# Performance work log

Hardware: AMD Instinct MI355X
Metric: run time of the kernel (lower is better)

Reference implementation:

```python
import jax, jax.numpy as jnp
import numpy as np

IN_FEATURES = 8192
OUT_FEATURES = 8192
MAX_STATES = 100
THRESHOLD = MAX_STATES // 2  # 50
TRACE_DECAY = 0.8


def setup_inputs() -> dict:
    key = jax.random.key(0)
    k1, k2 = jax.random.split(key)
    # binary spike input in {0,1}
    spike_input = (jax.random.uniform(k1, (1, IN_FEATURES)) < 0.5).astype(jnp.float32)
    # synapse states initialized around the threshold, as in the torch buffer init
    synapse_states = jax.random.randint(
        k2, (OUT_FEATURES, IN_FEATURES), THRESHOLD - 5, THRESHOLD + 5
    ).astype(jnp.float32)
    membrane_potential = jnp.zeros((OUT_FEATURES,), jnp.float32)
    adaptive_threshold = jnp.ones((OUT_FEATURES,), jnp.float32)
    eligibility_trace = jnp.zeros((OUT_FEATURES, IN_FEATURES), jnp.float32)
    return {
        "spike_input": spike_input,
        "synapse_states": synapse_states,
        "membrane_potential": membrane_potential,
        "adaptive_threshold": adaptive_threshold,
        "eligibility_trace": eligibility_trace,
    }


def reference(spike_input, synapse_states, membrane_potential, adaptive_threshold, eligibility_trace):
    # ternary (binary) weight mask from synapse states
    w = (synapse_states > THRESHOLD).astype(jnp.float32)  # [out, in]
    x = spike_input.reshape(1, -1)                         # [1, in]
    # current = x @ w^T, flattened to [out] (batch must be 1)
    current = jnp.einsum("bi,oi->bo", x, w).reshape(-1)    # [out]
    # LIF membrane update
    v_mem = membrane_potential * 0.7 + current             # [out]
    spikes = (v_mem >= adaptive_threshold).astype(jnp.float32)
    # eligibility trace: decay + outer-product update
    new_trace = eligibility_trace * TRACE_DECAY + jnp.outer(spikes, x.reshape(-1))
    # post-spike reset with soft decay
    new_v_mem = v_mem * (1.0 - spikes) * 0.5
    return spikes, new_v_mem, new_trace
```

## Files before the change

### kernel.cpp

```cpp
#include <hip/hip_runtime.h>


#define IN_F 8192
#define OUT_F 8192
#define THR_F 50.0f
#define BLOCK 256
#define V4_PER_THREAD 8

typedef float f4 __attribute__((ext_vector_type(4)));

__global__ __launch_bounds__(BLOCK) void snn_fused_kernel(
    const float* __restrict__ x,
    const float* __restrict__ syn,
    const float* __restrict__ vmem_in,
    const float* __restrict__ thr,
    const float* __restrict__ trace_in,
    float* __restrict__ out_spikes,
    float* __restrict__ out_vmem,
    float* __restrict__ out_trace)
{
    const int o = blockIdx.x;
    const int tid = threadIdx.x;
    const size_t rowoff = (size_t)o * IN_F;

    const f4* __restrict__ syn4 = reinterpret_cast<const f4*>(syn + rowoff);
    const f4* __restrict__ x4   = reinterpret_cast<const f4*>(x);
    const f4* __restrict__ tr4  = reinterpret_cast<const f4*>(trace_in + rowoff);
    f4* __restrict__ ot4        = reinterpret_cast<f4*>(out_trace + rowoff);

    f4 tr[V4_PER_THREAD];
#pragma unroll
    for (int j = 0; j < V4_PER_THREAD; ++j) {
        const int idx = tid + j * BLOCK;
        tr[j] = __builtin_nontemporal_load(&tr4[idx]);
    }

    float partial = 0.0f;
#pragma unroll
    for (int j = 0; j < V4_PER_THREAD; ++j) {
        const int idx = tid + j * BLOCK;
        const f4 s  = syn4[idx];
        const f4 xv = x4[idx];
        partial += (s.x > THR_F) ? xv.x : 0.0f;
        partial += (s.y > THR_F) ? xv.y : 0.0f;
        partial += (s.z > THR_F) ? xv.z : 0.0f;
        partial += (s.w > THR_F) ? xv.w : 0.0f;
    }

#pragma unroll
    for (int off = 32; off > 0; off >>= 1)
        partial += __shfl_down(partial, off, 64);

    __shared__ float wsum[BLOCK / 64];
    __shared__ float s_spike;
    const int wid = tid >> 6;
    const int lane = tid & 63;
    if (lane == 0) wsum[wid] = partial;
    __syncthreads();

    if (tid == 0) {
        const float cur = wsum[0] + wsum[1] + wsum[2] + wsum[3];
        const float v = vmem_in[o] * 0.7f + cur;
        const float sp = (v >= thr[o]) ? 1.0f : 0.0f;
        out_spikes[o] = sp;
        out_vmem[o] = v * (1.0f - sp) * 0.5f;
        s_spike = sp;
    }
    __syncthreads();
    const float sp = s_spike;

#pragma unroll
    for (int j = 0; j < V4_PER_THREAD; ++j) {
        const int idx = tid + j * BLOCK;
        const f4 xv = x4[idx];
        f4 r;
        r.x = tr[j].x * 0.8f + sp * xv.x;
        r.y = tr[j].y * 0.8f + sp * xv.y;
        r.z = tr[j].z * 0.8f + sp * xv.z;
        r.w = tr[j].w * 0.8f + sp * xv.w;
        __builtin_nontemporal_store(r, &ot4[idx]);
    }
}

extern "C" void kernel_launch(void* const* d_in, const int* in_sizes, int n_in,
                              void* d_out, int out_size, void* d_ws, size_t ws_size,
                              hipStream_t stream) {
    const float* x     = (const float*)d_in[0];
    const float* syn   = (const float*)d_in[1];
    const float* vmem  = (const float*)d_in[2];
    const float* thr   = (const float*)d_in[3];
    const float* trace = (const float*)d_in[4];

    float* out = (float*)d_out;
    float* out_spikes = out;
    float* out_vmem   = out + OUT_F;
    float* out_trace  = out + 2 * OUT_F;

    snn_fused_kernel<<<OUT_F, BLOCK, 0, stream>>>(
        x, syn, vmem, thr, trace, out_spikes, out_vmem, out_trace);
}
```

Measured before the change: 119.0 us.

## Assign one output row per wavefront and stream trace in chunks

Each wavefront now handles a whole output row instead of a block per row. This removes the shared-memory reduction and both block barriers, using an xor shuffle and a lane-0 broadcast instead. Synapse loads become nontemporal and run in chunks. Only the first trace chunk is prefetched before the spike decision, and the rest is streamed afterwards to keep register use down. Each wave now carries more serial work per row and fewer memory requests are in flight before the reduction.

```diff
diff --git a/kernel.cpp b/kernel.cpp
--- a/kernel.cpp
+++ b/kernel.cpp
@@ -5,11 +5,13 @@
 #define OUT_F 8192
 #define THR_F 50.0f
 #define BLOCK 256
-#define V4_PER_THREAD 8
+#define WAVES_PER_BLOCK 4
+#define CHUNK 8
+#define NCHUNK 4
 
 typedef float f4 __attribute__((ext_vector_type(4)));
 
-__global__ __launch_bounds__(BLOCK) void snn_fused_kernel(
+__global__ __launch_bounds__(BLOCK) void snn_wave_kernel(
     const float* __restrict__ x,
     const float* __restrict__ syn,
     const float* __restrict__ vmem_in,
@@ -19,8 +21,9 @@
     float* __restrict__ out_vmem,
     float* __restrict__ out_trace)
 {
-    const int o = blockIdx.x;
-    const int tid = threadIdx.x;
+    const int wid  = threadIdx.x >> 6;
+    const int lane = threadIdx.x & 63;
+    const int o    = blockIdx.x * WAVES_PER_BLOCK + wid;
     const size_t rowoff = (size_t)o * IN_F;
 
     const f4* __restrict__ syn4 = reinterpret_cast<const f4*>(syn + rowoff);
@@ -28,57 +31,73 @@
     const f4* __restrict__ tr4  = reinterpret_cast<const f4*>(trace_in + rowoff);
     f4* __restrict__ ot4        = reinterpret_cast<f4*>(out_trace + rowoff);
 
-    f4 tr[V4_PER_THREAD];
+    float partial = 0.0f;
 #pragma unroll
-    for (int j = 0; j < V4_PER_THREAD; ++j) {
-        const int idx = tid + j * BLOCK;
-        tr[j] = __builtin_nontemporal_load(&tr4[idx]);
+    for (int c = 0; c < NCHUNK; ++c) {
+        f4 s[CHUNK], xv[CHUNK];
+#pragma unroll
+        for (int j = 0; j < CHUNK; ++j) {
+            const int idx = lane + (c * CHUNK + j) * 64;
+            s[j]  = __builtin_nontemporal_load(&syn4[idx]);
+            xv[j] = x4[idx];
+        }
+#pragma unroll
+        for (int j = 0; j < CHUNK; ++j) {
+            partial += (s[j].x > THR_F) ? xv[j].x : 0.0f;
+            partial += (s[j].y > THR_F) ? xv[j].y : 0.0f;
+            partial += (s[j].z > THR_F) ? xv[j].z : 0.0f;
+            partial += (s[j].w > THR_F) ? xv[j].w : 0.0f;
+        }
     }
 
-    float partial = 0.0f;
+    f4 tpre[CHUNK];
 #pragma unroll
-    for (int j = 0; j < V4_PER_THREAD; ++j) {
-        const int idx = tid + j * BLOCK;
-        const f4 s  = syn4[idx];
-        const f4 xv = x4[idx];
-        partial += (s.x > THR_F) ? xv.x : 0.0f;
-        partial += (s.y > THR_F) ? xv.y : 0.0f;
-        partial += (s.z > THR_F) ? xv.z : 0.0f;
-        partial += (s.w > THR_F) ? xv.w : 0.0f;
-    }
+    for (int j = 0; j < CHUNK; ++j)
+        tpre[j] = __builtin_nontemporal_load(&tr4[lane + j * 64]);
 
 #pragma unroll
     for (int off = 32; off > 0; off >>= 1)
-        partial += __shfl_down(partial, off, 64);
+        partial += __shfl_xor(partial, off, 64);
 
-    __shared__ float wsum[BLOCK / 64];
-    __shared__ float s_spike;
-    const int wid = tid >> 6;
-    const int lane = tid & 63;
-    if (lane == 0) wsum[wid] = partial;
-    __syncthreads();
-
-    if (tid == 0) {
-        const float cur = wsum[0] + wsum[1] + wsum[2] + wsum[3];
-        const float v = vmem_in[o] * 0.7f + cur;
-        const float sp = (v >= thr[o]) ? 1.0f : 0.0f;
+    float sp;
+    if (lane == 0) {
+        const float v = vmem_in[o] * 0.7f + partial;
+        sp = (v >= thr[o]) ? 1.0f : 0.0f;
         out_spikes[o] = sp;
-        out_vmem[o] = v * (1.0f - sp) * 0.5f;
-        s_spike = sp;
+        out_vmem[o]   = v * (1.0f - sp) * 0.5f;
     }
-    __syncthreads();
-    const float sp = s_spike;
+    sp = __shfl(sp, 0, 64);
 
 #pragma unroll
-    for (int j = 0; j < V4_PER_THREAD; ++j) {
-        const int idx = tid + j * BLOCK;
+    for (int j = 0; j < CHUNK; ++j) {
+        const int idx = lane + j * 64;
         const f4 xv = x4[idx];
         f4 r;
-        r.x = tr[j].x * 0.8f + sp * xv.x;
-        r.y = tr[j].y * 0.8f + sp * xv.y;
-        r.z = tr[j].z * 0.8f + sp * xv.z;
-        r.w = tr[j].w * 0.8f + sp * xv.w;
+        r.x = tpre[j].x * 0.8f + sp * xv.x;
+        r.y = tpre[j].y * 0.8f + sp * xv.y;
+        r.z = tpre[j].z * 0.8f + sp * xv.z;
+        r.w = tpre[j].w * 0.8f + sp * xv.w;
         __builtin_nontemporal_store(r, &ot4[idx]);
+    }
+#pragma unroll
+    for (int c = 1; c < NCHUNK; ++c) {
+        f4 t[CHUNK], xv[CHUNK];
+#pragma unroll
+        for (int j = 0; j < CHUNK; ++j) {
+            const int idx = lane + (c * CHUNK + j) * 64;
+            t[j]  = __builtin_nontemporal_load(&tr4[idx]);
+            xv[j] = x4[idx];
+        }
+#pragma unroll
+        for (int j = 0; j < CHUNK; ++j) {
+            const int idx = lane + (c * CHUNK + j) * 64;
+            f4 r;
+            r.x = t[j].x * 0.8f + sp * xv[j].x;
+            r.y = t[j].y * 0.8f + sp * xv[j].y;
+            r.z = t[j].z * 0.8f + sp * xv[j].z;
+            r.w = t[j].w * 0.8f + sp * xv[j].w;
+            __builtin_nontemporal_store(r, &ot4[idx]);
+        }
     }
 }
 
@@ -96,6 +115,6 @@
     float* out_vmem   = out + OUT_F;
     float* out_trace  = out + 2 * OUT_F;
 
-    snn_fused_kernel<<<OUT_F, BLOCK, 0, stream>>>(
+    snn_wave_kernel<<<OUT_F / WAVES_PER_BLOCK, BLOCK, 0, stream>>>(
         x, syn, vmem, thr, trace, out_spikes, out_vmem, out_trace);
 }
```

New measurement: 134.6 us. 1.13x slower.

## Software-pipeline rows so trace update of row r-1 overlaps dot of row r

Applied to the files above, without the earlier changes.

Each block now processes four output rows and, in each step, interleaves the dot product for row r with the trace decay-and-update for row r-1, reusing the spike computed in the previous step. Grid size drops by four and the per-block serial phase (dot, then barrier, then trace) is replaced by a skewed pipeline, so trace loads and stores run alongside synapse loads. Every thread now reads the reduced spike from a double-buffered shared array instead of thread 0 broadcasting it. The catch is fewer blocks, plus trace loads that are no longer nontemporal and no longer issued ahead in registers.

```diff
diff --git a/kernel.cpp b/kernel.cpp
--- a/kernel.cpp
+++ b/kernel.cpp
@@ -5,11 +5,12 @@
 #define OUT_F 8192
 #define THR_F 50.0f
 #define BLOCK 256
-#define V4_PER_THREAD 8
+#define RPB 4
+#define NCHUNK 8
 
 typedef float f4 __attribute__((ext_vector_type(4)));
 
-__global__ __launch_bounds__(BLOCK) void snn_fused_kernel(
+__global__ __launch_bounds__(BLOCK) void snn_pipe_kernel(
     const float* __restrict__ x,
     const float* __restrict__ syn,
     const float* __restrict__ vmem_in,
@@ -19,66 +20,67 @@
     float* __restrict__ out_vmem,
     float* __restrict__ out_trace)
 {
-    const int o = blockIdx.x;
-    const int tid = threadIdx.x;
-    const size_t rowoff = (size_t)o * IN_F;
+    const int tid  = threadIdx.x;
+    const int base = blockIdx.x * RPB;
+    const f4* __restrict__ x4 = reinterpret_cast<const f4*>(x);
 
-    const f4* __restrict__ syn4 = reinterpret_cast<const f4*>(syn + rowoff);
-    const f4* __restrict__ x4   = reinterpret_cast<const f4*>(x);
-    const f4* __restrict__ tr4  = reinterpret_cast<const f4*>(trace_in + rowoff);
-    f4* __restrict__ ot4        = reinterpret_cast<f4*>(out_trace + rowoff);
+    __shared__ float wsum[2][4];
 
-    f4 tr[V4_PER_THREAD];
-#pragma unroll
-    for (int j = 0; j < V4_PER_THREAD; ++j) {
-        const int idx = tid + j * BLOCK;
-        tr[j] = __builtin_nontemporal_load(&tr4[idx]);
-    }
-
-    float partial = 0.0f;
-#pragma unroll
-    for (int j = 0; j < V4_PER_THREAD; ++j) {
-        const int idx = tid + j * BLOCK;
-        const f4 s  = syn4[idx];
-        const f4 xv = x4[idx];
-        partial += (s.x > THR_F) ? xv.x : 0.0f;
-        partial += (s.y > THR_F) ? xv.y : 0.0f;
-        partial += (s.z > THR_F) ? xv.z : 0.0f;
-        partial += (s.w > THR_F) ? xv.w : 0.0f;
-    }
+    float sp_prev = 0.0f;
 
 #pragma unroll
-    for (int off = 32; off > 0; off >>= 1)
-        partial += __shfl_down(partial, off, 64);
+    for (int r = 0; r <= RPB; ++r) {
+        const bool do_dot = (r < RPB);
+        const bool do_tr  = (r > 0);
+        const int  dot_row = base + (do_dot ? r : 0);
+        const int  tr_row  = base + (do_tr ? (r - 1) : 0);
 
-    __shared__ float wsum[BLOCK / 64];
-    __shared__ float s_spike;
-    const int wid = tid >> 6;
-    const int lane = tid & 63;
-    if (lane == 0) wsum[wid] = partial;
-    __syncthreads();
+        const f4* __restrict__ syn4 =
+            reinterpret_cast<const f4*>(syn + (size_t)dot_row * IN_F);
+        const f4* __restrict__ tr4 =
+            reinterpret_cast<const f4*>(trace_in + (size_t)tr_row * IN_F);
+        f4* __restrict__ ot4 =
+            reinterpret_cast<f4*>(out_trace + (size_t)tr_row * IN_F);
 
-    if (tid == 0) {
-        const float cur = wsum[0] + wsum[1] + wsum[2] + wsum[3];
-        const float v = vmem_in[o] * 0.7f + cur;
-        const float sp = (v >= thr[o]) ? 1.0f : 0.0f;
-        out_spikes[o] = sp;
-        out_vmem[o] = v * (1.0f - sp) * 0.5f;
-        s_spike = sp;
-    }
-    __syncthreads();
-    const float sp = s_spike;
+        float partial = 0.0f;
+#pragma unroll
+        for (int c = 0; c < NCHUNK; ++c) {
+            const int idx = tid + c * BLOCK;
+            const f4 xv = x4[idx];
+            if (do_dot) {
+                const f4 s = syn4[idx];
+                partial += (s.x > THR_F) ? xv.x : 0.0f;
+                partial += (s.y > THR_F) ? xv.y : 0.0f;
+                partial += (s.z > THR_F) ? xv.z : 0.0f;
+                partial += (s.w > THR_F) ? xv.w : 0.0f;
+            }
+            if (do_tr) {
+                const f4 t = tr4[idx];
+                f4 res;
+                res.x = t.x * 0.8f + sp_prev * xv.x;
+                res.y = t.y * 0.8f + sp_prev * xv.y;
+                res.z = t.z * 0.8f + sp_prev * xv.z;
+                res.w = t.w * 0.8f + sp_prev * xv.w;
+                __builtin_nontemporal_store(res, &ot4[idx]);
+            }
+        }
 
+        if (do_dot) {
 #pragma unroll
-    for (int j = 0; j < V4_PER_THREAD; ++j) {
-        const int idx = tid + j * BLOCK;
-        const f4 xv = x4[idx];
-        f4 r;
-        r.x = tr[j].x * 0.8f + sp * xv.x;
-        r.y = tr[j].y * 0.8f + sp * xv.y;
-        r.z = tr[j].z * 0.8f + sp * xv.z;
-        r.w = tr[j].w * 0.8f + sp * xv.w;
-        __builtin_nontemporal_store(r, &ot4[idx]);
+            for (int off = 32; off > 0; off >>= 1)
+                partial += __shfl_xor(partial, off, 64);
+            if ((tid & 63) == 0) wsum[r & 1][tid >> 6] = partial;
+            __syncthreads();
+            const float cur = wsum[r & 1][0] + wsum[r & 1][1] +
+                              wsum[r & 1][2] + wsum[r & 1][3];
+            const float v  = vmem_in[dot_row] * 0.7f + cur;
+            const float sp = (v >= thr[dot_row]) ? 1.0f : 0.0f;
+            if (tid == 0) {
+                out_spikes[dot_row] = sp;
+                out_vmem[dot_row]   = v * (1.0f - sp) * 0.5f;
+            }
+            sp_prev = sp;
+        }
     }
 }
 
@@ -96,6 +98,6 @@
     float* out_vmem   = out + OUT_F;
     float* out_trace  = out + 2 * OUT_F;
 
-    snn_fused_kernel<<<OUT_F, BLOCK, 0, stream>>>(
+    snn_pipe_kernel<<<OUT_F / RPB, BLOCK, 0, stream>>>(
         x, syn, vmem, thr, trace, out_spikes, out_vmem, out_trace);
 }
```

New measurement: 155.3 us. +30.5%, slower.
